# Performance work log

Hardware: AMD Instinct MI355X
Metric: run time of the kernel (lower is better)

Reference implementation:

```python
import jax, jax.numpy as jnp
import numpy as np

B = 16384
INPUT_DIM = 720
SEQ = 15
EMB = 6
OUT = 48
CIN = INPUT_DIM // SEQ      # 48
MID = INPUT_DIM // 3        # 240
PAD = (SEQ - 1) // 2        # 7 -> 'same' length output
WINDOW = SEQ / 50.0         # 0.3
TPI = 2.0 * np.pi
EPS = 1e-5


def conv1d(x, w, b):
    # x: [B, Cin, S], w: [Cout, Cin, K] -> [B, Cout, S]
    y = jax.lax.conv_general_dilated(x, w, (1,), [(PAD, PAD)],
                                     dimension_numbers=('NCH', 'OIH', 'NCH'))
    return y + b[None, :, None]


def layernorm(x, w, b):
    m = jnp.mean(x, axis=-1, keepdims=True)
    v = jnp.mean((x - m) ** 2, axis=-1, keepdims=True)
    return (x - m) * jax.lax.rsqrt(v + EPS) * w + b


def setup_inputs() -> dict:
    key = jax.random.key(0)
    ks = jax.random.split(key, 16)
    s = 0.05
    f32 = jnp.float32
    return {
        'x': jax.random.normal(ks[0], (B, INPUT_DIM), f32),
        'conv1_w': jax.random.normal(ks[1], (MID, CIN, SEQ), f32) * s,
        'conv1_b': jax.random.normal(ks[2], (MID,), f32) * s,
        'norm1_w': jnp.ones((MID * SEQ,), f32),
        'norm1_b': jnp.zeros((MID * SEQ,), f32),
        'conv2_w': jax.random.normal(ks[3], (EMB, MID, SEQ), f32) * s,
        'conv2_b': jax.random.normal(ks[4], (EMB,), f32) * s,
        'fc_w': jax.random.normal(ks[5], (EMB, 2, SEQ), f32) * s,
        'fc_b': jax.random.normal(ks[6], (EMB, 2), f32) * s,
        'deconv1_w': jax.random.normal(ks[7], (MID, EMB, SEQ), f32) * s,
        'deconv1_b': jax.random.normal(ks[8], (MID,), f32) * s,
        'denorm1_w': jnp.ones((MID * SEQ,), f32),
        'denorm1_b': jnp.zeros((MID * SEQ,), f32),
        'deconv2_w': jax.random.normal(ks[9], (OUT, MID, SEQ), f32) * s,
        'deconv2_b': jax.random.normal(ks[10], (OUT,), f32) * s,
    }


def reference(x, conv1_w, conv1_b, norm1_w, norm1_b, conv2_w, conv2_b,
              fc_w, fc_b, deconv1_w, deconv1_b, denorm1_w, denorm1_b,
              deconv2_w, deconv2_b):
    freqs = (jnp.fft.rfftfreq(SEQ)[1:] * SEQ / WINDOW).astype(jnp.float32)  # [7]
    args = jnp.linspace(-WINDOW / 2, WINDOW / 2, SEQ, dtype=jnp.float32)    # [15]

    h = x.reshape(B, CIN, SEQ)
    h = conv1d(h, conv1_w, conv1_b)                                  # [B,MID,S]
    h = layernorm(h.reshape(B, -1), norm1_w, norm1_b).reshape(B, MID, SEQ)
    h = jax.nn.elu(h)
    h = conv1d(h, conv2_w, conv2_b)                                  # [B,EMB,S]

    # FFT phase/amp/offset extraction along time axis
    rf = jnp.fft.rfft(h, axis=2)                                     # [B,EMB,8]
    power = jnp.abs(rf[:, :, 1:]) ** 2                               # [B,EMB,7]
    psum = jnp.sum(power, axis=2)
    f = jnp.sum(freqs * power, axis=2) / psum                        # [B,EMB]
    a = 2.0 * jnp.sqrt(psum) / SEQ                                   # [B,EMB]
    off = rf.real[:, :, 0] / SEQ                                     # [B,EMB]

    # per-embedding Linear(SEQ,2) + atan2 phase (vectorized over embeddings)
    v = jnp.einsum('bes,eos->beo', h, fc_w) + fc_b                   # [B,EMB,2]
    p = jnp.arctan2(v[..., 1], v[..., 0]) / TPI                      # [B,EMB]

    # sinusoid reconstruction
    sig = a[..., None] * jnp.sin(TPI * (f[..., None] * args + p[..., None])) + off[..., None]

    h = conv1d(sig, deconv1_w, deconv1_b)                            # [B,MID,S]
    h = layernorm(h.reshape(B, -1), denorm1_w, denorm1_b).reshape(B, MID, SEQ)
    h = jax.nn.elu(h)
    h = conv1d(h, deconv2_w, deconv2_b)                              # [B,OUT,S]
    return h[:, :, -1].reshape(B, -1)
```

## Files before the change

kernel.cpp:

```cpp
#include <hip/hip_runtime.h>

typedef _Float16 f16;
typedef _Float16 f16x8 __attribute__((ext_vector_type(8)));
typedef _Float16 f16x4 __attribute__((ext_vector_type(4)));
typedef float floatx4 __attribute__((ext_vector_type(4)));

#define TPI 6.283185307179586f
#define WSCALE 256.0f
#define INV_WSCALE (1.0f / 256.0f)

__device__ __forceinline__ void llds16(const f16* g, f16* l)
{
    __builtin_amdgcn_global_load_lds(
        (const __attribute__((address_space(1))) unsigned int*)g,
        (__attribute__((address_space(3))) unsigned int*)l, 16, 0, 0);
}

__global__ void prep_xh(const float* __restrict__ x, f16* __restrict__ Xh)
{
    const int TT = 8192 * 96;
    for (int i = blockIdx.x * 256 + threadIdx.x; i < TT; i += gridDim.x * 256) {
        int r = i / 96, g = (i - r * 96) * 8;
        f16x8 o = {};
        if (g < 720) {
            const float* xp = x + (size_t)r * 720 + g;
            float4 v0 = *(const float4*)xp;
            float4 v1 = *(const float4*)(xp + 4);
            o = (f16x8){(f16)v0.x, (f16)v0.y, (f16)v0.z, (f16)v0.w,
                        (f16)v1.x, (f16)v1.y, (f16)v1.z, (f16)v1.w};
        }
        *(f16x8*)(Xh + (size_t)r * 768 + g) = o;
    }
}

__global__ void prep_w(const float* __restrict__ w1, const float* __restrict__ w2,
                       const float* __restrict__ dw1, const float* __restrict__ dw2,
                       f16* __restrict__ B2,
                       f16* __restrict__ W2h, f16* __restrict__ W2l,
                       f16* __restrict__ D1, f16* __restrict__ D2)
{
    const int T1 = 3712 * 768;
    const int T2 = 96 * 3648;
    const int T3 = 3712 * 96;
    const int T4 = 48 * 3648;
    const int TT = T1 + T2 + T3 + T4;
    for (int i = blockIdx.x * 256 + threadIdx.x; i < TT; i += gridDim.x * 256) {
        if (i < T1) {
            int n = i / 768, k = i - n * 768;
            float v = 0.f;
            if (n < 3600 && k < 720) {
                int o = n / 15, t = n - o * 15, c = k / 15, s = k - c * 15, d = s - t + 7;
                if (d >= 0 && d < 15) v = w1[(o * 48 + c) * 15 + d];
            }
            v *= WSCALE;
            f16 hi = (f16)v;
            f16* row = B2 + (size_t)n * 1536 + k;
            row[0] = hi;
            row[768] = (f16)(v - (float)hi);
        } else if (i < T1 + T2) {
            int j = i - T1;
            int n = j / 3648, k = j - n * 3648;
            float v = 0.f;
            if (n < 90 && k < 3600) {
                int e = n / 15, t = n - e * 15, m = k / 15, s = k - m * 15, d = s - t + 7;
                if (d >= 0 && d < 15) v = w2[(e * 240 + m) * 15 + d];
            }
            v *= WSCALE;
            f16 hi = (f16)v;
            W2h[j] = hi; W2l[j] = (f16)(v - (float)hi);
        } else if (i < T1 + T2 + T3) {
            int j = i - T1 - T2;
            int n = j / 96, k = j - n * 96;
            float v = 0.f;
            if (n < 3600 && k < 90) {
                int m = n / 15, t = n - m * 15, e = k / 15, s = k - e * 15, d = s - t + 7;
                if (d >= 0 && d < 15) v = dw1[(m * 6 + e) * 15 + d];
            }
            D1[j] = (f16)v;
        } else {
            int j = i - T1 - T2 - T3;
            int o = j / 3648, k = j - o * 3648;
            float v = 0.f;
            if (k < 3600) {
                int m = k / 15, s = k - m * 15;
                if (s >= 7) v = dw2[(o * 240 + m) * 15 + (s - 7)];
            }
            D2[j] = (f16)v;
        }
    }
}

__global__ __launch_bounds__(256, 3) void gemm1_async(
    const f16* __restrict__ Xh, const f16* __restrict__ B2,
    float* __restrict__ H1, const float* __restrict__ bias,
    float* __restrict__ ssum, float* __restrict__ ssq, int m0)
{
    const int tid = threadIdx.x;
    const int wave = tid >> 6, lane = tid & 63;
    const int l15 = lane & 15, q = lane >> 4;
    const int wm = wave >> 1, wn = wave & 1;
    const int bm = blockIdx.x * 128, bn = blockIdx.y * 128;

    __shared__ __align__(16) f16 Asw[128 * 64];
    __shared__ __align__(16) f16 Bsw[2][128 * 64];

    floatx4 acc[4][4];
#pragma unroll
    for (int i = 0; i < 4; i++)
#pragma unroll
        for (int j = 0; j < 4; j++) acc[i][j] = (floatx4){0.f, 0.f, 0.f, 0.f};

    for (int kt = 0; kt < 12; kt++) {
        const int k0 = kt * 64;
#pragma unroll
        for (int it = 0; it < 4; it++) {
            int c = it * 256 + tid;
            int row = c >> 3;
            int seg = (c & 7) ^ (row & 7);
            llds16(Xh + (size_t)(bm + row) * 768 + k0 + seg * 8, &Asw[0] + (size_t)c * 8);
            const f16* gb = B2 + (size_t)(bn + row) * 1536 + k0 + seg * 8;
            llds16(gb,       &Bsw[0][0] + (size_t)c * 8);
            llds16(gb + 768, &Bsw[1][0] + (size_t)c * 8);
        }
        __syncthreads();
#pragma unroll
        for (int ks = 0; ks < 2; ks++) {
            f16x8 a[4], bh[4], bl[4];
#pragma unroll
            for (int i = 0; i < 4; i++) {
                int row = wm * 64 + i * 16 + l15;
                a[i] = *(const f16x8*)&Asw[row * 64 + (((ks * 4 + q) ^ (row & 7)) << 3)];
            }
#pragma unroll
            for (int jj = 0; jj < 4; jj++) {
                int row = wn * 64 + jj * 16 + l15;
                int off = row * 64 + (((ks * 4 + q) ^ (row & 7)) << 3);
                bh[jj] = *(const f16x8*)&Bsw[0][off];
                bl[jj] = *(const f16x8*)&Bsw[1][off];
            }
#pragma unroll
            for (int i = 0; i < 4; i++)
#pragma unroll
                for (int jj = 0; jj < 4; jj++) {
                    acc[i][jj] = __builtin_amdgcn_mfma_f32_16x16x32_f16(a[i], bh[jj], acc[i][jj], 0, 0, 0);
                    acc[i][jj] = __builtin_amdgcn_mfma_f32_16x16x32_f16(a[i], bl[jj], acc[i][jj], 0, 0, 0);
                }
        }
        __syncthreads();
    }

#pragma unroll
    for (int i = 0; i < 4; i++) {
#pragma unroll
        for (int ii = 0; ii < 4; ii++) {
            const int rg = m0 + bm + wm * 64 + i * 16 + q * 4 + ii;
            float s = 0.f, s2 = 0.f;
#pragma unroll
            for (int jj = 0; jj < 4; jj++) {
                const int cg = bn + wn * 64 + jj * 16 + l15;
                float v = acc[i][jj][ii] * INV_WSCALE;
                if (cg < 3600) {
                    v += bias[cg / 15];
                    H1[(size_t)rg * 3600 + cg] = v;
                } else v = 0.f;
                s += v; s2 += v * v;
            }
#pragma unroll
            for (int off = 1; off < 16; off <<= 1) {
                s += __shfl_xor(s, off);
                s2 += __shfl_xor(s2, off);
            }
            if (l15 == 0) {
                atomicAdd(&ssum[rg], s);
                atomicAdd(&ssq[rg], s2);
            }
        }
    }
}

__global__ __launch_bounds__(256) void conv2_pk(
    const float* __restrict__ H1, const f16* __restrict__ Bh, const f16* __restrict__ Bl,
    const float* __restrict__ ssum, const float* __restrict__ ssq,
    const float* __restrict__ lnw, const float* __restrict__ lnb,
    float* __restrict__ h2)
{
    const int tid = threadIdx.x;
    const int wave = tid >> 6, lane = tid & 63;
    const int l15 = lane & 15, q = lane >> 4;
    const int wm = wave >> 1, wn = wave & 1;
    const int bm = blockIdx.x * 128;
    const int chunk = blockIdx.y;
    const int t0 = (chunk == 0) ? 0 : 15 + 14 * (chunk - 1);
    const int nt = (chunk == 0) ? 15 : 14;

    __shared__ __align__(16) f16 Ah[128][88];
    __shared__ __align__(16) f16 Al[128][88];
    __shared__ __align__(16) f16 Bsw[2][96 * 64];
    __shared__ float mur[128], rsr[128];

    if (tid < 128) {
        float mu = ssum[bm + tid] * (1.f / 3600.f);
        float var = ssq[bm + tid] * (1.f / 3600.f) - mu * mu;
        mur[tid] = mu;
        rsr[tid] = rsqrtf(fmaxf(var, 0.f) + 1e-5f);
    }
    __syncthreads();

    floatx4 acc[4][3];
#pragma unroll
    for (int i = 0; i < 4; i++)
#pragma unroll
        for (int j = 0; j < 3; j++) acc[i][j] = (floatx4){0.f, 0.f, 0.f, 0.f};

    for (int t = 0; t < nt; t++) {
        const int k0 = (t0 + t) * 64;
#pragma unroll
        for (int it = 0; it < 3; it++) {
            int c = it * 256 + tid;
            int row = c >> 3;
            int seg = (c & 7) ^ (row & 7);
            llds16(Bh + (size_t)row * 3648 + k0 + seg * 8, &Bsw[0][0] + (size_t)c * 8);
            llds16(Bl + (size_t)row * 3648 + k0 + seg * 8, &Bsw[1][0] + (size_t)c * 8);
        }
#pragma unroll
        for (int it = 0; it < 8; it++) {
            int idx = it * 256 + tid;
            int r = idx >> 4, c4 = (idx & 15) * 4;
            int gc = k0 + c4;
            f16x4 hv = {(f16)0.f, (f16)0.f, (f16)0.f, (f16)0.f};
            f16x4 lv = hv;
            if (gc < 3600) {
                float4 v  = *(const float4*)(H1 + (size_t)(bm + r) * 3600 + gc);
                float4 w4 = *(const float4*)(lnw + gc);
                float4 b4 = *(const float4*)(lnb + gc);
                float mu = mur[r], rs = rsr[r];
                float z0 = (v.x - mu) * rs * w4.x + b4.x; z0 = z0 > 0.f ? z0 : (__expf(z0) - 1.f);
                float z1 = (v.y - mu) * rs * w4.y + b4.y; z1 = z1 > 0.f ? z1 : (__expf(z1) - 1.f);
                float z2 = (v.z - mu) * rs * w4.z + b4.z; z2 = z2 > 0.f ? z2 : (__expf(z2) - 1.f);
                float z3 = (v.w - mu) * rs * w4.w + b4.w; z3 = z3 > 0.f ? z3 : (__expf(z3) - 1.f);
                f16 h0 = (f16)z0, h1 = (f16)z1, h2v = (f16)z2, h3v = (f16)z3;
                hv = (f16x4){h0, h1, h2v, h3v};
                lv = (f16x4){(f16)(z0 - (float)h0), (f16)(z1 - (float)h1),
                             (f16)(z2 - (float)h2v), (f16)(z3 - (float)h3v)};
            }
            *(f16x4*)&Ah[r][c4] = hv;
            *(f16x4*)&Al[r][c4] = lv;
        }
        __syncthreads();
#pragma unroll
        for (int ks = 0; ks < 2; ks++) {
            f16x8 ah[4], al[4], bh[3], bl[3];
#pragma unroll
            for (int i = 0; i < 4; i++) {
                ah[i] = *(const f16x8*)&Ah[wm * 64 + i * 16 + l15][ks * 32 + q * 8];
                al[i] = *(const f16x8*)&Al[wm * 64 + i * 16 + l15][ks * 32 + q * 8];
            }
#pragma unroll
            for (int j = 0; j < 3; j++) {
                int row = wn * 48 + j * 16 + l15;
                int off = row * 64 + (((ks * 4 + q) ^ (row & 7)) << 3);
                bh[j] = *(const f16x8*)&Bsw[0][off];
                bl[j] = *(const f16x8*)&Bsw[1][off];
            }
#pragma unroll
            for (int i = 0; i < 4; i++)
#pragma unroll
                for (int j = 0; j < 3; j++) {
                    acc[i][j] = __builtin_amdgcn_mfma_f32_16x16x32_f16(ah[i], bh[j], acc[i][j], 0, 0, 0);
                    acc[i][j] = __builtin_amdgcn_mfma_f32_16x16x32_f16(al[i], bh[j], acc[i][j], 0, 0, 0);
                    acc[i][j] = __builtin_amdgcn_mfma_f32_16x16x32_f16(ah[i], bl[j], acc[i][j], 0, 0, 0);
                }
        }
        __syncthreads();
    }

#pragma unroll
    for (int i = 0; i < 4; i++)
#pragma unroll
        for (int ii = 0; ii < 4; ii++) {
            const int rg = bm + wm * 64 + i * 16 + q * 4 + ii;
#pragma unroll
            for (int j = 0; j < 3; j++) {
                const int cg = wn * 48 + j * 16 + l15;
                atomicAdd(&h2[(size_t)rg * 96 + cg], acc[i][j][ii]);
            }
        }
}

__global__ void extract(const float* __restrict__ h2, const float* __restrict__ c2b,
                        const float* __restrict__ fcw, const float* __restrict__ fcb,
                        f16* __restrict__ sig)
{
    __shared__ float ct[7][15], st[7][15], fw[180], fb[12];
    const int tid = threadIdx.x;
    if (tid < 105) {
        int kk = tid / 15, t = tid - kk * 15;
        double ang = (2.0 * 3.141592653589793 / 15.0) * (double)((kk + 1) * t);
        ct[kk][t] = (float)cos(ang);
        st[kk][t] = (float)sin(ang);
    }
    if (tid < 180) fw[tid] = fcw[tid];
    if (tid < 12) fb[tid] = fcb[tid];
    __syncthreads();

    const int task = blockIdx.x * 256 + tid;
    const int r = task / 6, e = task - (task / 6) * 6;
    float h[15];
    float mean = 0.f;
#pragma unroll
    for (int t = 0; t < 15; t++) {
        h[t] = h2[(size_t)r * 96 + e * 15 + t] * INV_WSCALE + c2b[e];
        mean += h[t];
    }
    mean *= (1.f / 15.f);
    float psum = 0.f, fsum = 0.f;
#pragma unroll
    for (int kk = 0; kk < 7; kk++) {
        float re = 0.f, im = 0.f;
#pragma unroll
        for (int t = 0; t < 15; t++) { re += h[t] * ct[kk][t]; im -= h[t] * st[kk][t]; }
        float p = re * re + im * im;
        psum += p;
        fsum += p * ((float)(kk + 1) * (10.f / 3.f));
    }
    float f = fsum / psum;
    float a = 2.f * sqrtf(psum) * (1.f / 15.f);
    float v0 = fb[e * 2 + 0], v1 = fb[e * 2 + 1];
#pragma unroll
    for (int t = 0; t < 15; t++) {
        v0 += h[t] * fw[(e * 2 + 0) * 15 + t];
        v1 += h[t] * fw[(e * 2 + 1) * 15 + t];
    }
    float ph = atan2f(v1, v0) * (1.f / TPI);
    f16* outp = sig + (size_t)r * 96 + e * 15;
#pragma unroll
    for (int t = 0; t < 15; t++) {
        float arg = f * (-0.15f + (float)t * (0.3f / 14.f)) + ph;
        outp[t] = (f16)(a * sinpif(2.f * arg) + mean);
    }
    if (e == 0) {
#pragma unroll
        for (int p2 = 0; p2 < 6; p2++) sig[(size_t)r * 96 + 90 + p2] = (f16)0.f;
    }
}

template <int BM, int BN, int BK, int WM, int WN>
__global__ __launch_bounds__(256) void gemm_k(
    const f16* __restrict__ A, int lda,
    const f16* __restrict__ B, int ldb,
    f16* __restrict__ C, int ldc, int K,
    const float* __restrict__ bias,
    int ncols_real, int ncols_store,
    float* __restrict__ ssum, float* __restrict__ ssq)
{
    constexpr int WN_N = BN / WN;
    constexpr int MT = WM / 16, NT = WN / 16;
    constexpr int SEG = BK / 8;
    const int tid = threadIdx.x;
    const int wave = tid >> 6, lane = tid & 63;
    const int l15 = lane & 15, q = lane >> 4;
    const int wm = wave / WN_N, wn = wave % WN_N;
    const int bm = blockIdx.x * BM;
    const int bn = blockIdx.y * BN;

    __shared__ __align__(16) f16 As[BM][BK + 8];
    __shared__ __align__(16) f16 Bs[BN][BK + 8];

    floatx4 acc[MT][NT];
#pragma unroll
    for (int i = 0; i < MT; i++)
#pragma unroll
        for (int j = 0; j < NT; j++) acc[i][j] = (floatx4){0.f, 0.f, 0.f, 0.f};

    for (int k0 = 0; k0 < K; k0 += BK) {
        for (int idx = tid; idx < BM * SEG; idx += 256) {
            int r = idx / SEG, s = idx - r * SEG;
            *(uint4*)(&As[r][s * 8]) = *(const uint4*)(A + (size_t)(bm + r) * lda + k0 + s * 8);
        }
        for (int idx = tid; idx < BN * SEG; idx += 256) {
            int r = idx / SEG, s = idx - r * SEG;
            *(uint4*)(&Bs[r][s * 8]) = *(const uint4*)(B + (size_t)(bn + r) * ldb + k0 + s * 8);
        }
        __syncthreads();
#pragma unroll
        for (int ks = 0; ks < BK / 32; ks++) {
            f16x8 af[MT], bf[NT];
#pragma unroll
            for (int i = 0; i < MT; i++)
                af[i] = *(const f16x8*)(&As[wm * WM + i * 16 + l15][ks * 32 + q * 8]);
#pragma unroll
            for (int j = 0; j < NT; j++)
                bf[j] = *(const f16x8*)(&Bs[wn * WN + j * 16 + l15][ks * 32 + q * 8]);
#pragma unroll
            for (int i = 0; i < MT; i++)
#pragma unroll
                for (int j = 0; j < NT; j++)
                    acc[i][j] = __builtin_amdgcn_mfma_f32_16x16x32_f16(af[i], bf[j], acc[i][j], 0, 0, 0);
        }
        __syncthreads();
    }

#pragma unroll
    for (int i = 0; i < MT; i++) {
#pragma unroll
        for (int ii = 0; ii < 4; ii++) {
            const int rg = bm + wm * WM + i * 16 + q * 4 + ii;
            float s = 0.f, s2 = 0.f;
#pragma unroll
            for (int j = 0; j < NT; j++) {
                const int cg = bn + wn * WN + j * 16 + l15;
                float v = acc[i][j][ii];
                if (cg < ncols_real) v += bias[cg / 15]; else v = 0.f;
                if (cg < ncols_store) C[(size_t)rg * ldc + cg] = (f16)v;
                s += v; s2 += v * v;
            }
#pragma unroll
            for (int off = 1; off < 16; off <<= 1) {
                s += __shfl_xor(s, off);
                s2 += __shfl_xor(s2, off);
            }
            if (l15 == 0) {
                atomicAdd(&ssum[rg], s);
                atomicAdd(&ssq[rg], s2);
            }
        }
    }
}

__global__ __launch_bounds__(256) void deconv2_ln(
    const f16* __restrict__ h3, const f16* __restrict__ D2,
    const float* __restrict__ ssum, const float* __restrict__ ssq,
    const float* __restrict__ lnw, const float* __restrict__ lnb,
    const float* __restrict__ bias, float* __restrict__ out)
{
    const int tid = threadIdx.x;
    const int wave = tid >> 6, lane = tid & 63;
    const int l15 = lane & 15, q = lane >> 4;
    const int bm = blockIdx.x * 64;
    const int chunk = blockIdx.y;
    const int t0 = (chunk == 0) ? 0 : 15 + 14 * (chunk - 1);
    const int nt = (chunk == 0) ? 15 : 14;

    __shared__ __align__(16) f16 As[64][88];
    __shared__ __align__(16) f16 Bs[48][88];
    __shared__ float mur[64], rsr[64];

    if (tid < 64) {
        float mu = ssum[bm + tid] * (1.f / 3600.f);
        float var = ssq[bm + tid] * (1.f / 3600.f) - mu * mu;
        mur[tid] = mu;
        rsr[tid] = rsqrtf(fmaxf(var, 0.f) + 1e-5f);
    }
    __syncthreads();

    floatx4 acc[3];
#pragma unroll
    for (int j = 0; j < 3; j++) acc[j] = (floatx4){0.f, 0.f, 0.f, 0.f};

    for (int t = 0; t < nt; t++) {
        const int k0 = (t0 + t) * 64;
#pragma unroll
        for (int it = 0; it < 2; it++) {
            int idx = it * 256 + tid;
            int r = idx >> 3, s = idx & 7;
            int gc = k0 + s * 8;
            f16x8 o = {};
            if (gc < 3600) {
                f16x8 v = *(const f16x8*)(h3 + (size_t)(bm + r) * 3648 + gc);
                float mu = mur[r], rs = rsr[r];
#pragma unroll
                for (int e = 0; e < 8; e++) {
                    float y = ((float)v[e] - mu) * rs * lnw[gc + e] + lnb[gc + e];
                    o[e] = (f16)(y > 0.f ? y : (__expf(y) - 1.f));
                }
            }
            *(f16x8*)&As[r][s * 8] = o;
        }
        for (int idx = tid; idx < 384; idx += 256) {
            int r = idx >> 3, s = idx & 7;
            *(uint4*)&Bs[r][s * 8] = *(const uint4*)(D2 + (size_t)r * 3648 + k0 + s * 8);
        }
        __syncthreads();
#pragma unroll
        for (int ks = 0; ks < 2; ks++) {
            f16x8 a = *(const f16x8*)&As[wave * 16 + l15][ks * 32 + q * 8];
#pragma unroll
            for (int j = 0; j < 3; j++) {
                f16x8 b = *(const f16x8*)&Bs[j * 16 + l15][ks * 32 + q * 8];
                acc[j] = __builtin_amdgcn_mfma_f32_16x16x32_f16(a, b, acc[j], 0, 0, 0);
            }
        }
        __syncthreads();
    }

#pragma unroll
    for (int j = 0; j < 3; j++)
#pragma unroll
        for (int ii = 0; ii < 4; ii++) {
            int rg = bm + wave * 16 + q * 4 + ii;
            int cg = j * 16 + l15;
            float v = acc[j][ii];
            if (chunk == 0) v += bias[cg];
            atomicAdd(&out[(size_t)rg * 48 + cg], v);
        }
}

extern "C" void kernel_launch(void* const* d_in, const int* in_sizes, int n_in,
                              void* d_out, int out_size, void* d_ws, size_t ws_size,
                              hipStream_t stream)
{
    const float* x   = (const float*)d_in[0];
    const float* w1  = (const float*)d_in[1];
    const float* b1  = (const float*)d_in[2];
    const float* nw1 = (const float*)d_in[3];
    const float* nb1 = (const float*)d_in[4];
    const float* w2  = (const float*)d_in[5];
    const float* b2  = (const float*)d_in[6];
    const float* fcw = (const float*)d_in[7];
    const float* fcb = (const float*)d_in[8];
    const float* dw1 = (const float*)d_in[9];
    const float* db1 = (const float*)d_in[10];
    const float* nw2 = (const float*)d_in[11];
    const float* nb2 = (const float*)d_in[12];
    const float* dw2 = (const float*)d_in[13];
    const float* db2 = (const float*)d_in[14];
    float* out = (float*)d_out;

    f16* B2  = (f16*)d_ws;
    f16* W2h = B2  + (size_t)3712 * 1536;
    f16* W2l = W2h + (size_t)96 * 3648;
    f16* D1  = W2l + (size_t)96 * 3648;
    f16* D2  = D1  + (size_t)3712 * 96;
    float* stats = (float*)(D2 + (size_t)48 * 3648);
    float* s1 = stats;
    float* q1 = stats + 16384;
    float* s3 = stats + 32768;
    float* q3 = stats + 49152;
    float* h2 = stats + 4 * 16384;
    f16* sigb = (f16*)(h2 + (size_t)16384 * 96);
    f16* Xh   = (f16*)h2;
    float* H1 = (float*)((char*)h2 + 12582912);
    f16* h3   = (f16*)H1;

    hipMemsetAsync(stats, 0, (size_t)4 * 16384 * 4, stream);
    hipMemsetAsync(out, 0, (size_t)16384 * 48 * 4, stream);

    prep_w<<<2048, 256, 0, stream>>>(w1, w2, dw1, dw2, B2, W2h, W2l, D1, D2);

    prep_xh<<<1536, 256, 0, stream>>>(x, Xh);
    gemm1_async<<<dim3(64, 29), 256, 0, stream>>>(Xh, B2, H1, b1, s1, q1, 0);
    prep_xh<<<1536, 256, 0, stream>>>(x + (size_t)8192 * 720, Xh);
    gemm1_async<<<dim3(64, 29), 256, 0, stream>>>(Xh, B2, H1, b1, s1, q1, 8192);

    hipMemsetAsync(h2, 0, (size_t)16384 * 96 * 4, stream);

    conv2_pk<<<dim3(128, 4), 256, 0, stream>>>(H1, W2h, W2l, s1, q1, nw1, nb1, h2);

    extract<<<384, 256, 0, stream>>>(h2, b2, fcw, fcb, sigb);

    gemm_k<128, 128, 96, 64, 64><<<dim3(128, 29), 256, 0, stream>>>(
        sigb, 96, D1, 96, h3, 3648, 96, db1, 3600, 3648, s3, q3);

    deconv2_ln<<<dim3(256, 4), 256, 0, stream>>>(h3, D2, s3, q3, nw2, nb2, db2, out);
}
```

Baseline: 668.5 us.

## Fuse deconv1, layernorm, ELU and deconv2 by recomputing deconv1 instead of storing it

The deconv1 GEMM no longer writes its 16384x3648 f16 intermediate. A stats-only pass computes the per-row layernorm sums. A fused kernel then recomputes the deconv1 tile, applies layernorm and ELU in registers/LDS, and feeds the result straight into the deconv2 MFMA, writing the output directly instead of through atomics. This removes a large round trip through global memory and the output memset, at the cost of computing the deconv1 GEMM twice. Each of the two kernels launches only 256 blocks and has a serialized sync-heavy loop over 57 or 29 K tiles, so occupancy may suffer.

Result: slower. 701.3 us (+4.9%).

```diff
diff --git a/kernel.cpp b/kernel.cpp
--- a/kernel.cpp
+++ b/kernel.cpp
@@ -117,7 +117,7 @@
             int c = it * 256 + tid;
             int row = c >> 3;
             int seg = (c & 7) ^ (row & 7);
-            llds16(Xh + (size_t)(bm + row) * 768 + k0 + seg * 8, &Asw[0] + (size_t)c * 8);
+            llds16(Xh + (size_t)(bm + row) * 768 + k0 + seg * 8, Asw + (size_t)c * 8);
             const f16* gb = B2 + (size_t)(bn + row) * 1536 + k0 + seg * 8;
             llds16(gb,       &Bsw[0][0] + (size_t)c * 8);
             llds16(gb + 768, &Bsw[1][0] + (size_t)c * 8);
@@ -344,105 +344,94 @@
     }
 }
 
-template <int BM, int BN, int BK, int WM, int WN>
-__global__ __launch_bounds__(256) void gemm_k(
-    const f16* __restrict__ A, int lda,
-    const f16* __restrict__ B, int ldb,
-    f16* __restrict__ C, int ldc, int K,
-    const float* __restrict__ bias,
-    int ncols_real, int ncols_store,
-    float* __restrict__ ssum, float* __restrict__ ssq)
-{
-    constexpr int WN_N = BN / WN;
-    constexpr int MT = WM / 16, NT = WN / 16;
-    constexpr int SEG = BK / 8;
+__global__ __launch_bounds__(256) void deconv1_stats(
+    const f16* __restrict__ sigb, const f16* __restrict__ D1,
+    const float* __restrict__ bias, float* __restrict__ ssum, float* __restrict__ ssq)
+{
     const int tid = threadIdx.x;
-    const int wave = tid >> 6, lane = tid & 63;
+    const int w = tid >> 6, lane = tid & 63;
     const int l15 = lane & 15, q = lane >> 4;
-    const int wm = wave / WN_N, wn = wave % WN_N;
-    const int bm = blockIdx.x * BM;
-    const int bn = blockIdx.y * BN;
-
-    __shared__ __align__(16) f16 As[BM][BK + 8];
-    __shared__ __align__(16) f16 Bs[BN][BK + 8];
-
-    floatx4 acc[MT][NT];
-#pragma unroll
-    for (int i = 0; i < MT; i++)
-#pragma unroll
-        for (int j = 0; j < NT; j++) acc[i][j] = (floatx4){0.f, 0.f, 0.f, 0.f};
-
-    for (int k0 = 0; k0 < K; k0 += BK) {
-        for (int idx = tid; idx < BM * SEG; idx += 256) {
-            int r = idx / SEG, s = idx - r * SEG;
-            *(uint4*)(&As[r][s * 8]) = *(const uint4*)(A + (size_t)(bm + r) * lda + k0 + s * 8);
-        }
-        for (int idx = tid; idx < BN * SEG; idx += 256) {
-            int r = idx / SEG, s = idx - r * SEG;
-            *(uint4*)(&Bs[r][s * 8]) = *(const uint4*)(B + (size_t)(bn + r) * ldb + k0 + s * 8);
-        }
-        __syncthreads();
-#pragma unroll
-        for (int ks = 0; ks < BK / 32; ks++) {
-            f16x8 af[MT], bf[NT];
-#pragma unroll
-            for (int i = 0; i < MT; i++)
-                af[i] = *(const f16x8*)(&As[wm * WM + i * 16 + l15][ks * 32 + q * 8]);
-#pragma unroll
-            for (int j = 0; j < NT; j++)
-                bf[j] = *(const f16x8*)(&Bs[wn * WN + j * 16 + l15][ks * 32 + q * 8]);
-#pragma unroll
-            for (int i = 0; i < MT; i++)
-#pragma unroll
-                for (int j = 0; j < NT; j++)
-                    acc[i][j] = __builtin_amdgcn_mfma_f32_16x16x32_f16(af[i], bf[j], acc[i][j], 0, 0, 0);
-        }
-        __syncthreads();
-    }
-
-#pragma unroll
-    for (int i = 0; i < MT; i++) {
-#pragma unroll
-        for (int ii = 0; ii < 4; ii++) {
-            const int rg = bm + wm * WM + i * 16 + q * 4 + ii;
-            float s = 0.f, s2 = 0.f;
-#pragma unroll
-            for (int j = 0; j < NT; j++) {
-                const int cg = bn + wn * WN + j * 16 + l15;
-                float v = acc[i][j][ii];
-                if (cg < ncols_real) v += bias[cg / 15]; else v = 0.f;
-                if (cg < ncols_store) C[(size_t)rg * ldc + cg] = (f16)v;
-                s += v; s2 += v * v;
-            }
-#pragma unroll
-            for (int off = 1; off < 16; off <<= 1) {
-                s += __shfl_xor(s, off);
-                s2 += __shfl_xor(s2, off);
-            }
-            if (l15 == 0) {
-                atomicAdd(&ssum[rg], s);
-                atomicAdd(&ssq[rg], s2);
-            }
-        }
-    }
-}
-
-__global__ __launch_bounds__(256) void deconv2_ln(
-    const f16* __restrict__ h3, const f16* __restrict__ D2,
+    const int bm = blockIdx.x * 64;
+
+    __shared__ __align__(16) f16 As[64][104];
+    __shared__ __align__(16) f16 Bs[128][104];
+
+#pragma unroll
+    for (int it = 0; it < 3; it++) {
+        int c = it * 256 + tid;
+        int r = c / 12, s = c - r * 12;
+        *(uint4*)&As[r][s * 8] = *(const uint4*)(sigb + (size_t)(bm + r) * 96 + s * 8);
+    }
+
+    float sa[4] = {0.f, 0.f, 0.f, 0.f}, qa[4] = {0.f, 0.f, 0.f, 0.f};
+
+    for (int bn = 0; bn < 3712; bn += 128) {
+        __syncthreads();
+#pragma unroll
+        for (int it = 0; it < 6; it++) {
+            int c = it * 256 + tid;
+            int r = c / 12, s = c - r * 12;
+            *(uint4*)&Bs[r][s * 8] = *(const uint4*)(D1 + (size_t)(bn + r) * 96 + s * 8);
+        }
+        __syncthreads();
+
+        floatx4 acc[8];
+#pragma unroll
+        for (int j = 0; j < 8; j++) acc[j] = (floatx4){0.f, 0.f, 0.f, 0.f};
+#pragma unroll
+        for (int ks = 0; ks < 3; ks++) {
+            f16x8 a = *(const f16x8*)&As[w * 16 + l15][ks * 32 + q * 8];
+#pragma unroll
+            for (int j = 0; j < 8; j++) {
+                f16x8 b = *(const f16x8*)&Bs[j * 16 + l15][ks * 32 + q * 8];
+                acc[j] = __builtin_amdgcn_mfma_f32_16x16x32_f16(a, b, acc[j], 0, 0, 0);
+            }
+        }
+#pragma unroll
+        for (int j = 0; j < 8; j++) {
+            const int cg = bn + j * 16 + l15;
+            if (cg < 3600) {
+                float bv = bias[cg / 15];
+#pragma unroll
+                for (int ii = 0; ii < 4; ii++) {
+                    float v = acc[j][ii] + bv;
+                    sa[ii] += v; qa[ii] += v * v;
+                }
+            }
+        }
+    }
+
+#pragma unroll
+    for (int ii = 0; ii < 4; ii++) {
+#pragma unroll
+        for (int off = 1; off < 16; off <<= 1) {
+            sa[ii] += __shfl_xor(sa[ii], off);
+            qa[ii] += __shfl_xor(qa[ii], off);
+        }
+        if (l15 == 0) {
+            const int rg = bm + w * 16 + q * 4 + ii;
+            ssum[rg] = sa[ii];
+            ssq[rg]  = qa[ii];
+        }
+    }
+}
+
+__global__ __launch_bounds__(256) void fused_deconv(
+    const f16* __restrict__ sigb, const f16* __restrict__ D1, const f16* __restrict__ D2,
     const float* __restrict__ ssum, const float* __restrict__ ssq,
     const float* __restrict__ lnw, const float* __restrict__ lnb,
-    const float* __restrict__ bias, float* __restrict__ out)
+    const float* __restrict__ b1, const float* __restrict__ b2,
+    float* __restrict__ out)
 {
     const int tid = threadIdx.x;
-    const int wave = tid >> 6, lane = tid & 63;
+    const int w = tid >> 6, lane = tid & 63;
     const int l15 = lane & 15, q = lane >> 4;
     const int bm = blockIdx.x * 64;
-    const int chunk = blockIdx.y;
-    const int t0 = (chunk == 0) ? 0 : 15 + 14 * (chunk - 1);
-    const int nt = (chunk == 0) ? 15 : 14;
-
-    __shared__ __align__(16) f16 As[64][88];
-    __shared__ __align__(16) f16 Bs[48][88];
+
+    __shared__ __align__(16) f16 As[64][104];
+    __shared__ __align__(16) f16 D1s[64][104];
+    __shared__ __align__(16) f16 hs[64][72];
+    __shared__ __align__(16) f16 D2s[48][72];
     __shared__ float mur[64], rsr[64];
 
     if (tid < 64) {
@@ -451,57 +440,79 @@
         mur[tid] = mu;
         rsr[tid] = rsqrtf(fmaxf(var, 0.f) + 1e-5f);
     }
-    __syncthreads();
-
-    floatx4 acc[3];
-#pragma unroll
-    for (int j = 0; j < 3; j++) acc[j] = (floatx4){0.f, 0.f, 0.f, 0.f};
-
-    for (int t = 0; t < nt; t++) {
-        const int k0 = (t0 + t) * 64;
-#pragma unroll
-        for (int it = 0; it < 2; it++) {
-            int idx = it * 256 + tid;
-            int r = idx >> 3, s = idx & 7;
-            int gc = k0 + s * 8;
-            f16x8 o = {};
-            if (gc < 3600) {
-                f16x8 v = *(const f16x8*)(h3 + (size_t)(bm + r) * 3648 + gc);
-                float mu = mur[r], rs = rsr[r];
-#pragma unroll
-                for (int e = 0; e < 8; e++) {
-                    float y = ((float)v[e] - mu) * rs * lnw[gc + e] + lnb[gc + e];
-                    o[e] = (f16)(y > 0.f ? y : (__expf(y) - 1.f));
+#pragma unroll
+    for (int it = 0; it < 3; it++) {
+        int c = it * 256 + tid;
+        int r = c / 12, s = c - r * 12;
+        *(uint4*)&As[r][s * 8] = *(const uint4*)(sigb + (size_t)(bm + r) * 96 + s * 8);
+    }
+
+    floatx4 acc_out[3];
+#pragma unroll
+    for (int j = 0; j < 3; j++) acc_out[j] = (floatx4){0.f, 0.f, 0.f, 0.f};
+
+    for (int kt = 0; kt < 57; kt++) {
+        const int k0 = kt * 64;
+        __syncthreads();
+#pragma unroll
+        for (int it = 0; it < 3; it++) {
+            int c = it * 256 + tid;
+            int r = c / 12, s = c - r * 12;
+            *(uint4*)&D1s[r][s * 8] = *(const uint4*)(D1 + (size_t)(k0 + r) * 96 + s * 8);
+        }
+        for (int c = tid; c < 384; c += 256) {
+            int r = c >> 3, s = c & 7;
+            *(uint4*)&D2s[r][s * 8] = *(const uint4*)(D2 + (size_t)r * 3648 + k0 + s * 8);
+        }
+        __syncthreads();
+
+        floatx4 acc4[4];
+#pragma unroll
+        for (int i = 0; i < 4; i++) acc4[i] = (floatx4){0.f, 0.f, 0.f, 0.f};
+#pragma unroll
+        for (int ks = 0; ks < 3; ks++) {
+            f16x8 bt = *(const f16x8*)&D1s[w * 16 + l15][ks * 32 + q * 8];
+#pragma unroll
+            for (int i = 0; i < 4; i++) {
+                f16x8 at = *(const f16x8*)&As[i * 16 + l15][ks * 32 + q * 8];
+                acc4[i] = __builtin_amdgcn_mfma_f32_16x16x32_f16(at, bt, acc4[i], 0, 0, 0);
+            }
+        }
+        const int cg = k0 + w * 16 + l15;
+        float bv = (cg < 3600) ? b1[cg / 15] : 0.f;
+        float lw = (cg < 3600) ? lnw[cg] : 0.f;
+        float lb = (cg < 3600) ? lnb[cg] : 0.f;
+#pragma unroll
+        for (int i = 0; i < 4; i++)
+#pragma unroll
+            for (int ii = 0; ii < 4; ii++) {
+                const int m = i * 16 + q * 4 + ii;
+                f16 hv = (f16)0.f;
+                if (cg < 3600) {
+                    float y = (acc4[i][ii] + bv - mur[m]) * rsr[m] * lw + lb;
+                    hv = (f16)(y > 0.f ? y : (__expf(y) - 1.f));
                 }
-            }
-            *(f16x8*)&As[r][s * 8] = o;
-        }
-        for (int idx = tid; idx < 384; idx += 256) {
-            int r = idx >> 3, s = idx & 7;
-            *(uint4*)&Bs[r][s * 8] = *(const uint4*)(D2 + (size_t)r * 3648 + k0 + s * 8);
-        }
+                hs[m][w * 16 + l15] = hv;
+            }
         __syncthreads();
 #pragma unroll
         for (int ks = 0; ks < 2; ks++) {
-            f16x8 a = *(const f16x8*)&As[wave * 16 + l15][ks * 32 + q * 8];
+            f16x8 a = *(const f16x8*)&hs[w * 16 + l15][ks * 32 + q * 8];
 #pragma unroll
             for (int j = 0; j < 3; j++) {
-                f16x8 b = *(const f16x8*)&Bs[j * 16 + l15][ks * 32 + q * 8];
-                acc[j] = __builtin_amdgcn_mfma_f32_16x16x32_f16(a, b, acc[j], 0, 0, 0);
-            }
-        }
-        __syncthreads();
+                f16x8 b = *(const f16x8*)&D2s[j * 16 + l15][ks * 32 + q * 8];
+                acc_out[j] = __builtin_amdgcn_mfma_f32_16x16x32_f16(a, b, acc_out[j], 0, 0, 0);
+            }
+        }
     }
 
 #pragma unroll
     for (int j = 0; j < 3; j++)
 #pragma unroll
         for (int ii = 0; ii < 4; ii++) {
-            int rg = bm + wave * 16 + q * 4 + ii;
-            int cg = j * 16 + l15;
-            float v = acc[j][ii];
-            if (chunk == 0) v += bias[cg];
-            atomicAdd(&out[(size_t)rg * 48 + cg], v);
+            const int rg = bm + w * 16 + q * 4 + ii;
+            const int c = j * 16 + l15;
+            out[(size_t)rg * 48 + c] = acc_out[j][ii] + b2[c];
         }
 }
 
@@ -540,10 +551,8 @@
     f16* sigb = (f16*)(h2 + (size_t)16384 * 96);
     f16* Xh   = (f16*)h2;
     float* H1 = (float*)((char*)h2 + 12582912);
-    f16* h3   = (f16*)H1;
 
     hipMemsetAsync(stats, 0, (size_t)4 * 16384 * 4, stream);
-    hipMemsetAsync(out, 0, (size_t)16384 * 48 * 4, stream);
 
     prep_w<<<2048, 256, 0, stream>>>(w1, w2, dw1, dw2, B2, W2h, W2l, D1, D2);
 
@@ -558,8 +567,6 @@
 
     extract<<<384, 256, 0, stream>>>(h2, b2, fcw, fcb, sigb);
 
-    gemm_k<128, 128, 96, 64, 64><<<dim3(128, 29), 256, 0, stream>>>(
-        sigb, 96, D1, 96, h3, 3648, 96, db1, 3600, 3648, s3, q3);
-
-    deconv2_ln<<<dim3(256, 4), 256, 0, stream>>>(h3, D2, s3, q3, nw2, nb2, db2, out);
-}
+    deconv1_stats<<<256, 256, 0, stream>>>(sigb, D1, db1, s3, q3);
+    fused_deconv<<<256, 256, 0, stream>>>(sigb, D1, D2, s3, q3, nw2, nb2, db1, db2, out);
+}
```
